# Kernel optimization log

Measured on AMD Instinct MI355X. Metric: run time of the kernel, lower is better.

## Reference

```python
import jax, jax.numpy as jnp
import numpy as np

N_NODES = 50000
N_EDGES = 800000
IN_CH, HID_CH, OUT_CH = 128, 256, 256
N_LAYERS = 3


def setup_inputs() -> dict:
    key = jax.random.key(0)
    ks = jax.random.split(key, 9)
    x = jax.random.normal(ks[0], (N_NODES, IN_CH), dtype=jnp.float32)
    edge_index = jax.random.randint(ks[1], (2, N_EDGES), 0, N_NODES, dtype=jnp.int32)
    # Linear params, Kaiming-ish scale
    W1 = jax.random.normal(ks[2], (IN_CH, HID_CH), dtype=jnp.float32) / np.float32(np.sqrt(IN_CH))
    b1 = jnp.zeros((HID_CH,), jnp.float32)
    W2 = jax.random.normal(ks[3], (HID_CH, HID_CH), dtype=jnp.float32) / np.float32(np.sqrt(HID_CH))
    b2 = jnp.zeros((HID_CH,), jnp.float32)
    W3 = jax.random.normal(ks[4], (HID_CH, OUT_CH), dtype=jnp.float32) / np.float32(np.sqrt(HID_CH))
    b3 = jnp.zeros((OUT_CH,), jnp.float32)
    # learnable eps per GINConv (train_eps=True); small nonzero values for a nontrivial test
    eps = jax.random.normal(ks[5], (N_LAYERS,), dtype=jnp.float32) * 0.01
    return {"x": x, "edge_index": edge_index, "W1": W1, "b1": b1,
            "W2": W2, "b2": b2, "W3": W3, "b3": b3, "eps": eps}


def _gin_conv(x, src, dst, eps, W, b):
    # sum aggregation over incoming edges: agg[i] = sum_{(j->i)} x[j]
    agg = jax.ops.segment_sum(x[src], dst, num_segments=N_NODES)
    h = (1.0 + eps) * x + agg
    return h @ W + b


def reference(x, edge_index, W1, b1, W2, b2, W3, b3, eps):
    src, dst = edge_index[0], edge_index[1]
    # layers 0..L-2: conv -> relu -> dropout (identity in eval mode)
    h = jax.nn.relu(_gin_conv(x, src, dst, eps[0], W1, b1))
    h = jax.nn.relu(_gin_conv(h, src, dst, eps[1], W2, b2))
    # final layer: no relu
    out = _gin_conv(h, src, dst, eps[2], W3, b3)
    return out
```

## Files before the change

kernel.cpp:

```cpp
#include <hip/hip_runtime.h>


typedef __attribute__((ext_vector_type(8))) short short8;
typedef __attribute__((ext_vector_type(4))) float f32x4;

__device__ inline unsigned short f2bf(float f) {
    union { float f; unsigned u; } v; v.f = f;
    unsigned r = v.u + 0x7fffu + ((v.u >> 16) & 1u);
    return (unsigned short)(r >> 16);
}
__device__ inline float bflo(unsigned u) { return __uint_as_float(u << 16); }
__device__ inline float bfhi(unsigned u) { return __uint_as_float(u & 0xffff0000u); }

__device__ __forceinline__ void gload_lds16(const unsigned short* g, unsigned short* l) {
    __builtin_amdgcn_global_load_lds(
        (const __attribute__((address_space(1))) unsigned int*)g,
        (__attribute__((address_space(3))) unsigned int*)l,
        16, 0, 0);
}

#define ACC8(v) { acc[0]+=bflo(v.x); acc[1]+=bfhi(v.x); acc[2]+=bflo(v.y); acc[3]+=bfhi(v.y); \
                  acc[4]+=bflo(v.z); acc[5]+=bfhi(v.z); acc[6]+=bflo(v.w); acc[7]+=bfhi(v.w); }

__global__ __launch_bounds__(256) void prep_kernel(
    const float* __restrict__ x, const int* __restrict__ dst,
    const float* __restrict__ W1, const float* __restrict__ W2,
    const float* __restrict__ W3,
    unsigned short* __restrict__ xb, int* __restrict__ cnt,
    unsigned short* __restrict__ Ws1, unsigned short* __restrict__ Ws2,
    unsigned short* __restrict__ Ws3, int M, int nE)
{
    const int i  = blockIdx.x * 256 + threadIdx.x;
    const int nx = M * 16;
    if (i < nx) {
        const float4* xf = reinterpret_cast<const float4*>(x);
        float4 a = xf[2*i], b = xf[2*i + 1];
        uint4 o;
        o.x = (unsigned)f2bf(a.x) | ((unsigned)f2bf(a.y) << 16);
        o.y = (unsigned)f2bf(a.z) | ((unsigned)f2bf(a.w) << 16);
        o.z = (unsigned)f2bf(b.x) | ((unsigned)f2bf(b.y) << 16);
        o.w = (unsigned)f2bf(b.z) | ((unsigned)f2bf(b.w) << 16);
        reinterpret_cast<uint4*>(xb)[i] = o;
    } else if (i < nx + nE) {
        atomicAdd(&cnt[dst[i - nx]], 1);
    } else {
        int j = i - nx - nE;
        const float* W; unsigned short* D;
        if (j < 32768)       { W = W1; D = Ws1; }
        else if (j < 98304)  { W = W2; D = Ws2; j -= 32768; }
        else if (j < 163840) { W = W3; D = Ws3; j -= 98304; }
        else return;
        const int k = j >> 8, n = j & 255;
        D[((size_t)(k >> 3) * 256 + n) * 8 + (k & 7)] = f2bf(W[(size_t)k * 256 + n]);
    }
}


__global__ __launch_bounds__(1024) void scan1_kernel(
    const int* __restrict__ cnt, int* __restrict__ excl,
    int* __restrict__ bsum, int n)
{
    __shared__ int sh[1024];
    const int tid = threadIdx.x;
    const int i = blockIdx.x * 1024 + tid;
    int v = (i < n) ? cnt[i] : 0;
    sh[tid] = v;
    __syncthreads();
    #pragma unroll
    for (int off = 1; off < 1024; off <<= 1) {
        int t = (tid >= off) ? sh[tid - off] : 0;
        __syncthreads();
        sh[tid] += t;
        __syncthreads();
    }
    if (i < n) excl[i] = sh[tid] - v;
    if (tid == 1023) bsum[blockIdx.x] = sh[1023];
}

__global__ __launch_bounds__(1024) void scan3_kernel(
    const int* __restrict__ excl, const int* __restrict__ bsum,
    int* __restrict__ row_start, int* __restrict__ cursor,
    int n, int nE, int nbl)
{
    __shared__ int sb[64];
    const int tid = threadIdx.x;
    if (tid < 64) sb[tid] = (tid < nbl) ? bsum[tid] : 0;
    __syncthreads();
    #pragma unroll
    for (int off = 1; off < 64; off <<= 1) {
        int v = 0;
        if (tid < 64 && tid >= off) v = sb[tid - off];
        __syncthreads();
        if (tid < 64) sb[tid] += v;
        __syncthreads();
    }
    const int boff = sb[blockIdx.x] - bsum[blockIdx.x];
    const int i = blockIdx.x * 1024 + tid;
    if (i < n) {
        int v = excl[i] + boff;
        row_start[i] = v;
        cursor[i] = v;
    }
    if (i == 0) row_start[n] = nE;
}

__global__ __launch_bounds__(256) void build_adj_kernel(
    const int* __restrict__ src, const int* __restrict__ dst,
    int* __restrict__ cursor, int* __restrict__ adj, int nE)
{
    int e = blockIdx.x * 256 + threadIdx.x;
    if (e < nE) {
        int p = atomicAdd(&cursor[dst[e]], 1);
        adj[p] = src[e];
    }
}


template <int C>
__global__ __launch_bounds__(256) void aggregate_bf16(
    const unsigned short* __restrict__ X, const int* __restrict__ row_start,
    const int* __restrict__ adj, const float* __restrict__ eps_arr, int layer,
    unsigned short* __restrict__ H, int M)
{
    constexpr int TPN = C / 8;
    constexpr int NPB = 256 / TPN;
    const int node = blockIdx.x * NPB + (threadIdx.x / TPN);
    const int c8   = threadIdx.x & (TPN - 1);
    if (node >= M) return;

    const uint4* __restrict__ X4 = reinterpret_cast<const uint4*>(X);

    float acc[8] = {0.f,0.f,0.f,0.f,0.f,0.f,0.f,0.f};
    const int s0 = row_start[node];
    const int s1 = row_start[node + 1];

    int j = s0;
    for (; j + 3 < s1; j += 4) {
        int a0 = adj[j], a1 = adj[j+1], a2 = adj[j+2], a3 = adj[j+3];
        uint4 v0 = X4[(size_t)a0 * TPN + c8];
        uint4 v1 = X4[(size_t)a1 * TPN + c8];
        uint4 v2 = X4[(size_t)a2 * TPN + c8];
        uint4 v3 = X4[(size_t)a3 * TPN + c8];
        ACC8(v0); ACC8(v1); ACC8(v2); ACC8(v3);
    }
    for (; j < s1; ++j) {
        uint4 v = X4[(size_t)adj[j] * TPN + c8];
        ACC8(v);
    }

    const uint4 xv = X4[(size_t)node * TPN + c8];
    const float epsv = 1.0f + eps_arr[layer];
    float o[8];
    o[0] = epsv * bflo(xv.x) + acc[0]; o[1] = epsv * bfhi(xv.x) + acc[1];
    o[2] = epsv * bflo(xv.y) + acc[2]; o[3] = epsv * bfhi(xv.y) + acc[3];
    o[4] = epsv * bflo(xv.z) + acc[4]; o[5] = epsv * bfhi(xv.z) + acc[5];
    o[6] = epsv * bflo(xv.w) + acc[6]; o[7] = epsv * bfhi(xv.w) + acc[7];

    uint4 ov;
    ov.x = (unsigned)f2bf(o[0]) | ((unsigned)f2bf(o[1]) << 16);
    ov.y = (unsigned)f2bf(o[2]) | ((unsigned)f2bf(o[3]) << 16);
    ov.z = (unsigned)f2bf(o[4]) | ((unsigned)f2bf(o[5]) << 16);
    ov.w = (unsigned)f2bf(o[6]) | ((unsigned)f2bf(o[7]) << 16);
    reinterpret_cast<uint4*>(H)[(size_t)node * TPN + c8] = ov;
}


template <int CIN, int RELU, int BF16OUT>
__global__ __launch_bounds__(256) void gemm_tiled(
    const unsigned short* __restrict__ H, const unsigned short* __restrict__ Wsub,
    const float* __restrict__ bias, void* __restrict__ out, int M)
{
    constexpr int S = CIN / 32;

    __shared__ __align__(16) unsigned short As[4][64][8];

    const int t    = threadIdx.x;
    const int bm   = blockIdx.x * 64;
    const int w    = t >> 6, lane = t & 63;
    const int lr   = lane & 15, ko = lane >> 4;

    const int srow = t & 63;
    const unsigned short* aG = H + (size_t)(bm + srow) * CIN + (t >> 6) * 8;
    unsigned short* lA = &As[t >> 6][srow][0];

    f32x4 acc[4][4];
    #pragma unroll
    for (int fn = 0; fn < 4; ++fn) {
        const float bb = bias[w*64 + fn*16 + lr];
        #pragma unroll
        for (int fm = 0; fm < 4; ++fm) {
            acc[fm][fn][0] = bb; acc[fm][fn][1] = bb;
            acc[fm][fn][2] = bb; acc[fm][fn][3] = bb;
        }
    }

    for (int s = 0; s < S; ++s) {
        gload_lds16(aG + s*32, lA);
        __syncthreads();

        short8 af[4], bf8[4];
        #pragma unroll
        for (int fm = 0; fm < 4; ++fm)
            af[fm] = *reinterpret_cast<const short8*>(&As[ko][fm*16 + lr][0]);
        #pragma unroll
        for (int fn = 0; fn < 4; ++fn)
            bf8[fn] = *reinterpret_cast<const short8*>(
                Wsub + ((size_t)(s*4 + ko) * 256 + w*64 + fn*16 + lr) * 8);
        #pragma unroll
        for (int fm = 0; fm < 4; ++fm)
            #pragma unroll
            for (int fn = 0; fn < 4; ++fn)
                acc[fm][fn] = __builtin_amdgcn_mfma_f32_16x16x32_bf16(
                    af[fm], bf8[fn], acc[fm][fn], 0, 0, 0);

        __syncthreads();
    }

    #pragma unroll
    for (int fm = 0; fm < 4; ++fm) {
        #pragma unroll
        for (int fn = 0; fn < 4; ++fn) {
            const int col = w*64 + fn*16 + lr;
            #pragma unroll
            for (int r = 0; r < 4; ++r) {
                const int row = bm + fm*16 + ko*4 + r;
                if (row < M) {
                    float v = acc[fm][fn][r];
                    if (RELU) v = fmaxf(v, 0.f);
                    if (BF16OUT)
                        ((unsigned short*)out)[(size_t)row * 256 + col] = f2bf(v);
                    else
                        ((float*)out)[(size_t)row * 256 + col] = v;
                }
            }
        }
    }
}


extern "C" void kernel_launch(void* const* d_in, const int* in_sizes, int n_in,
                              void* d_out, int out_size, void* d_ws, size_t ws_size,
                              hipStream_t stream)
{
    const float* x   = (const float*)d_in[0];
    const int*   ei  = (const int*)  d_in[1];
    const float* W1  = (const float*)d_in[2];
    const float* b1  = (const float*)d_in[3];
    const float* W2  = (const float*)d_in[4];
    const float* b2  = (const float*)d_in[5];
    const float* W3  = (const float*)d_in[6];
    const float* b3  = (const float*)d_in[7];
    const float* eps = (const float*)d_in[8];

    const int M  = in_sizes[0] / 128;
    const int nE = in_sizes[1] / 2;
    const int Mp = ((M + 63) / 64) * 64;
    const int* srcI = ei;
    const int* dstI = ei + nE;

    char* p = (char*)d_ws;
    unsigned short* xb  = (unsigned short*)p; p += (size_t)Mp * 128 * 2;
    unsigned short* h1  = (unsigned short*)p; p += (size_t)Mp * 256 * 2;
    unsigned short* h2  = (unsigned short*)p; p += (size_t)Mp * 256 * 2;
    unsigned short* Ws1 = (unsigned short*)p; p += (size_t)128 * 256 * 2;
    unsigned short* Ws2 = (unsigned short*)p; p += (size_t)256 * 256 * 2;
    unsigned short* Ws3 = (unsigned short*)p; p += (size_t)256 * 256 * 2;
    int* cnt       = (int*)p; p += (size_t)M * 4;
    int* excl      = (int*)p; p += (size_t)M * 4;
    int* bsum      = (int*)p; p += 64 * 4;
    int* row_start = (int*)p; p += (size_t)(M + 2) * 4;
    int* cursor    = (int*)p; p += (size_t)M * 4;
    int* adj       = (int*)p; p += (size_t)nE * 4;

    const int nbl = (M + 1023) / 1024;

    hipMemsetAsync(cnt, 0, (size_t)M * sizeof(int), stream);
    {
        const int total = M * 16 + nE + 163840;
        prep_kernel<<<(total + 255) / 256, 256, 0, stream>>>(
            x, dstI, W1, W2, W3, xb, cnt, Ws1, Ws2, Ws3, M, nE);
    }
    scan1_kernel<<<nbl, 1024, 0, stream>>>(cnt, excl, bsum, M);
    scan3_kernel<<<nbl, 1024, 0, stream>>>(excl, bsum, row_start, cursor, M, nE, nbl);
    build_adj_kernel<<<(nE + 255) / 256, 256, 0, stream>>>(srcI, dstI, cursor, adj, nE);

    const int gblk = Mp / 64;

    aggregate_bf16<128><<<(M + 15) / 16, 256, 0, stream>>>(
        xb, row_start, adj, eps, 0, h1, M);
    gemm_tiled<128, 1, 1><<<gblk, 256, 0, stream>>>(h1, Ws1, b1, h2, M);

    aggregate_bf16<256><<<(M + 7) / 8, 256, 0, stream>>>(
        h2, row_start, adj, eps, 1, h1, M);
    gemm_tiled<256, 1, 1><<<gblk, 256, 0, stream>>>(h1, Ws2, b2, h2, M);

    aggregate_bf16<256><<<(M + 7) / 8, 256, 0, stream>>>(
        h2, row_start, adj, eps, 2, h1, M);
    gemm_tiled<256, 0, 0><<<gblk, 256, 0, stream>>>(h1, Ws3, b3, d_out, M);
}
```

Before: 301.8 us.

## Prefetch neighbor rows in aggregation and double-buffer LDS in GEMM

The aggregation loop is software-pipelined: it issues the next four neighbor-row loads before accumulating the previous four, so more gathers are in flight at once. The GEMM A-tile staging switches to a two-slot LDS buffer. The next k-slice is loaded asynchronously while the current one is consumed, which removes one barrier per iteration. The cost is more registers in the aggregation and twice the LDS in the GEMM. Overlap may be limited if vmcnt waits on the global weight loads also serialize the async LDS load.

```diff
diff --git a/kernel.cpp b/kernel.cpp
--- a/kernel.cpp
+++ b/kernel.cpp
@@ -133,15 +133,26 @@
     float acc[8] = {0.f,0.f,0.f,0.f,0.f,0.f,0.f,0.f};
     const int s0 = row_start[node];
     const int s1 = row_start[node + 1];
+    const int deg = s1 - s0;
 
     int j = s0;
-    for (; j + 3 < s1; j += 4) {
+    if (deg >= 4) {
+        const int jend = s0 + (deg & ~3);
         int a0 = adj[j], a1 = adj[j+1], a2 = adj[j+2], a3 = adj[j+3];
-        uint4 v0 = X4[(size_t)a0 * TPN + c8];
-        uint4 v1 = X4[(size_t)a1 * TPN + c8];
-        uint4 v2 = X4[(size_t)a2 * TPN + c8];
-        uint4 v3 = X4[(size_t)a3 * TPN + c8];
-        ACC8(v0); ACC8(v1); ACC8(v2); ACC8(v3);
+        uint4 p0 = X4[(size_t)a0 * TPN + c8];
+        uint4 p1 = X4[(size_t)a1 * TPN + c8];
+        uint4 p2 = X4[(size_t)a2 * TPN + c8];
+        uint4 p3 = X4[(size_t)a3 * TPN + c8];
+        for (j += 4; j < jend; j += 4) {
+            const int b0 = adj[j], b1 = adj[j+1], b2 = adj[j+2], b3 = adj[j+3];
+            const uint4 n0 = X4[(size_t)b0 * TPN + c8];
+            const uint4 n1 = X4[(size_t)b1 * TPN + c8];
+            const uint4 n2 = X4[(size_t)b2 * TPN + c8];
+            const uint4 n3 = X4[(size_t)b3 * TPN + c8];
+            ACC8(p0); ACC8(p1); ACC8(p2); ACC8(p3);
+            p0 = n0; p1 = n1; p2 = n2; p3 = n3;
+        }
+        ACC8(p0); ACC8(p1); ACC8(p2); ACC8(p3);
     }
     for (; j < s1; ++j) {
         uint4 v = X4[(size_t)adj[j] * TPN + c8];
@@ -172,7 +183,7 @@
 {
     constexpr int S = CIN / 32;
 
-    __shared__ __align__(16) unsigned short As[4][64][8];
+    __shared__ __align__(16) unsigned short As[2][4][64][8];
 
     const int t    = threadIdx.x;
     const int bm   = blockIdx.x * 64;
@@ -180,8 +191,8 @@
     const int lr   = lane & 15, ko = lane >> 4;
 
     const int srow = t & 63;
-    const unsigned short* aG = H + (size_t)(bm + srow) * CIN + (t >> 6) * 8;
-    unsigned short* lA = &As[t >> 6][srow][0];
+    const int skb  = t >> 6;
+    const unsigned short* aG = H + (size_t)(bm + srow) * CIN + skb * 8;
 
     f32x4 acc[4][4];
     #pragma unroll
@@ -194,14 +205,18 @@
         }
     }
 
+    gload_lds16(aG, &As[0][skb][srow][0]);
+
+    int cur = 0;
     for (int s = 0; s < S; ++s) {
-        gload_lds16(aG + s*32, lA);
-        __syncthreads();
+        __syncthreads();
+        if (s + 1 < S)
+            gload_lds16(aG + (s+1)*32, &As[cur ^ 1][skb][srow][0]);
 
         short8 af[4], bf8[4];
         #pragma unroll
         for (int fm = 0; fm < 4; ++fm)
-            af[fm] = *reinterpret_cast<const short8*>(&As[ko][fm*16 + lr][0]);
+            af[fm] = *reinterpret_cast<const short8*>(&As[cur][ko][fm*16 + lr][0]);
         #pragma unroll
         for (int fn = 0; fn < 4; ++fn)
             bf8[fn] = *reinterpret_cast<const short8*>(
@@ -213,7 +228,7 @@
                 acc[fm][fn] = __builtin_amdgcn_mfma_f32_16x16x32_bf16(
                     af[fm], bf8[fn], acc[fm][fn], 0, 0, 0);
 
-        __syncthreads();
+        cur ^= 1;
     }
 
     #pragma unroll
```

New measurement: 303.4 us. Within noise of the previous version (+0.5%).
